# Kernel optimization log

Measured on AMD Instinct MI355X. Metric: run time of the kernel, lower is better.

Reference implementation:

```python
import jax, jax.numpy as jnp
import numpy as np

F_FIELDS = 39
VOCAB = 200000
EMB = 16
D1 = 32
BATCH = 16384


def setup_inputs() -> dict:
    key = jax.random.key(0)
    ks = jax.random.split(key, 12)
    Xi = jax.random.randint(ks[0], (BATCH, F_FIELDS, 1), 0, VOCAB, dtype=jnp.int64 if jax.config.jax_enable_x64 else jnp.int32)
    Xv = jax.random.uniform(ks[1], (BATCH, F_FIELDS), dtype=jnp.float32)
    # one table per field, all same vocab -> stacked [F, V, E]
    tables = jax.random.normal(ks[2], (F_FIELDS, VOCAB, EMB), dtype=jnp.float32) * 0.05
    W1 = jax.random.normal(ks[3], (D1, F_FIELDS, EMB), dtype=jnp.float32)   # first_order_weight
    Wi = jax.random.normal(ks[4], (D1, F_FIELDS, EMB), dtype=jnp.float32)   # inner_second_weight_emb
    lin1_w = jax.random.normal(ks[5], (32, 32), dtype=jnp.float32) * (1.0 / np.sqrt(32))
    lin1_b = jax.random.normal(ks[6], (32,), dtype=jnp.float32) * 0.01
    lin2_w = jax.random.normal(ks[7], (32, 32), dtype=jnp.float32) * (1.0 / np.sqrt(32))
    lin2_b = jax.random.normal(ks[8], (32,), dtype=jnp.float32) * 0.01
    last_w = jax.random.normal(ks[9], (1, 32), dtype=jnp.float32) * (1.0 / np.sqrt(32))
    last_b = jax.random.normal(ks[10], (1,), dtype=jnp.float32) * 0.01
    return {"Xi": Xi, "Xv": Xv, "tables": tables, "W1": W1, "Wi": Wi,
            "lin1_w": lin1_w, "lin1_b": lin1_b, "lin2_w": lin2_w, "lin2_b": lin2_b,
            "last_w": last_w, "last_b": last_b}


def reference(Xi, Xv, tables, W1, Wi, lin1_w, lin1_b, lin2_w, lin2_b, last_w, last_b):
    # Per-field embedding lookup; Xi[:, f, 0] indexes field f's table.
    idx = Xi[:, :, 0]                                   # [B, F]
    emb = tables[jnp.arange(F_FIELDS)[None, :], idx]    # [B, F, E]
    emb = emb * Xv[:, :, None]                          # scale by feature value
    # first-order product layer: sum_j <emb_j, w_{i,j}> for each output unit i
    first_order = jnp.einsum('bfe,dfe->bd', emb, W1)    # [B, D1]
    # inner-product term: (sum_j <emb_j, wi_{i,j}>)^2
    s = jnp.einsum('bfe,dfe->bd', emb, Wi)
    x = first_order + s * s                             # [B, D1]
    # deep MLP (relu, eval mode: no dropout; bias param in original is unused in forward)
    x = jax.nn.relu(x @ lin1_w.T + lin1_b)
    x = jax.nn.relu(x @ lin2_w.T + lin2_b)
    out = x @ last_w.T + last_b                         # [B, 1]
    return jnp.sum(out, axis=1)                         # [B]
```

## Files before the change

### kernel.cpp

```cpp
#include <hip/hip_runtime.h>
#include <stdint.h>
#include <stddef.h>

#define F_FIELDS 39
#define VOCAB    200000
#define EMB      16
#define BATCH    16384
#define MBLK     32
#define NOUT     64
#define KPAD     640
#define NCHUNK   10
#define KC       64
#define ASTR     88
#define BSTR     88
#define CSTR     68

typedef __attribute__((ext_vector_type(8))) short bf16x8;
typedef __attribute__((ext_vector_type(4))) float f32x4;

__device__ __forceinline__ unsigned short f2bf(float x) {
  union { float f; unsigned int u; } a; a.f = x;
  unsigned int r = (a.u + 0x7fffu + ((a.u >> 16) & 1u)) >> 16;
  return (unsigned short)r;
}
__device__ __forceinline__ float bf2f(unsigned short h) {
  union { unsigned int u; float f; } a; a.u = ((unsigned int)h) << 16;
  return a.f;
}

__global__ void prep_w(const float* __restrict__ W1, const float* __restrict__ Wi,
                       unsigned short* __restrict__ Wt) {
  int i = blockIdx.x * 256 + threadIdx.x;
  if (i >= NOUT * KPAD) return;
  int n = i / KPAD, k = i % KPAD;
  float v = 0.0f;
  if (k < F_FIELDS * EMB) v = (n < 32) ? W1[n * 624 + k] : Wi[(n - 32) * 624 + k];
  Wt[i] = f2bf(v);
}

__global__ __launch_bounds__(256) void pnn_main(
    const int* __restrict__ Xi, const float* __restrict__ Xv,
    const float* __restrict__ tables, const unsigned short* __restrict__ Wt,
    const float* __restrict__ lin1_w, const float* __restrict__ lin1_b,
    const float* __restrict__ lin2_w, const float* __restrict__ lin2_b,
    const float* __restrict__ last_w, const float* __restrict__ last_b,
    float* __restrict__ out)
{
  const int t    = threadIdx.x;
  const int wave = t >> 6, lane = t & 63;
  const int l15  = lane & 15, quad = lane >> 4;

  __shared__ unsigned short A_sh[MBLK * ASTR];
  __shared__ unsigned short Al_sh[MBLK * ASTR];
  __shared__ unsigned short B_sh[NOUT * BSTR];
  __shared__ float          C_sh[MBLK * CSTR];
  __shared__ float          X1_sh[MBLK * 36];
  __shared__ float          W_lds[2145];

  for (int i = t; i < 1024; i += 256) {
    W_lds[i]        = lin1_w[i];
    W_lds[1024 + i] = lin2_w[i];
  }
  if (t < 32) {
    W_lds[2048 + t] = lin1_b[t];
    W_lds[2080 + t] = lin2_b[t];
    W_lds[2112 + t] = last_w[t];
  }
  if (t == 0) W_lds[2144] = last_b[0];

  const int gm    = t & 31;
  const int gfl   = (t >> 5) & 3;
  const int ghalf = t >> 7;
  const int sample = blockIdx.x * MBLK + gm;

  int   idxs[NCHUNK];
  float xvs[NCHUNK];
#pragma unroll
  for (int c = 0; c < NCHUNK; ++c) {
    int f = c * 4 + gfl;
    bool v = (f < F_FIELDS);
    int g = sample * F_FIELDS + (v ? f : 0);
    idxs[c] = v ? Xi[g] : 0;
    xvs[c]  = v ? Xv[g] : 0.0f;
  }

  const int bn = t >> 2, bseg = t & 3;

  const int m_tile = wave & 1, n_half = wave >> 1;
  const int arow = m_tile * 16 + l15;
  const int nb0  = n_half * 32 + l15;

  f32x4 acc0 = {0.f, 0.f, 0.f, 0.f};
  f32x4 acc1 = {0.f, 0.f, 0.f, 0.f};

#pragma unroll
  for (int c = 0; c < NCHUNK; ++c) {
    {
      const uint4* src = (const uint4*)(Wt + bn * KPAD + c * KC + bseg * 16);
      uint4 w0 = src[0], w1 = src[1];
      uint4* dst = (uint4*)&B_sh[bn * BSTR + bseg * 16];
      dst[0] = w0; dst[1] = w1;
    }
    {
      int f = c * 4 + gfl;
      float4 v0 = {0.f,0.f,0.f,0.f}, v1 = {0.f,0.f,0.f,0.f};
      float xv = xvs[c];
      if (f < F_FIELDS) {
        const float* p = tables + ((size_t)f * VOCAB + (size_t)idxs[c]) * EMB + ghalf * 8;
        v0 = *(const float4*)p;
        v1 = *(const float4*)(p + 4);
      }
      float vals[8] = { v0.x * xv, v0.y * xv, v0.z * xv, v0.w * xv,
                        v1.x * xv, v1.y * xv, v1.z * xv, v1.w * xv };
      union { unsigned short us[8]; uint4 v; } hi, lo;
#pragma unroll
      for (int j = 0; j < 8; ++j) {
        unsigned short h = f2bf(vals[j]);
        hi.us[j] = h;
        lo.us[j] = f2bf(vals[j] - bf2f(h));
      }
      *(uint4*)&A_sh[gm * ASTR + gfl * 16 + ghalf * 8]  = hi.v;
      *(uint4*)&Al_sh[gm * ASTR + gfl * 16 + ghalf * 8] = lo.v;
    }
    __syncthreads();
#pragma unroll
    for (int kk = 0; kk < 2; ++kk) {
      bf16x8 ah = *(const bf16x8*)&A_sh[arow * ASTR + kk * 32 + quad * 8];
      bf16x8 al = *(const bf16x8*)&Al_sh[arow * ASTR + kk * 32 + quad * 8];
      bf16x8 b0 = *(const bf16x8*)&B_sh[nb0 * BSTR + kk * 32 + quad * 8];
      bf16x8 b1 = *(const bf16x8*)&B_sh[(nb0 + 16) * BSTR + kk * 32 + quad * 8];
      acc0 = __builtin_amdgcn_mfma_f32_16x16x32_bf16(ah, b0, acc0, 0, 0, 0);
      acc1 = __builtin_amdgcn_mfma_f32_16x16x32_bf16(ah, b1, acc1, 0, 0, 0);
      acc0 = __builtin_amdgcn_mfma_f32_16x16x32_bf16(al, b0, acc0, 0, 0, 0);
      acc1 = __builtin_amdgcn_mfma_f32_16x16x32_bf16(al, b1, acc1, 0, 0, 0);
    }
    __syncthreads();
  }

  {
    int row_base = m_tile * 16 + quad * 4;
    int col0 = n_half * 32 + l15;
#pragma unroll
    for (int r = 0; r < 4; ++r) {
      C_sh[(row_base + r) * CSTR + col0]      = acc0[r];
      C_sh[(row_base + r) * CSTR + col0 + 16] = acc1[r];
    }
  }
  __syncthreads();

  {
    int m = t >> 3, j0 = (t & 7) * 4;
#pragma unroll
    for (int j = 0; j < 4; ++j) {
      float fo = C_sh[m * CSTR + j0 + j];
      float s  = C_sh[m * CSTR + 32 + j0 + j];
      C_sh[m * CSTR + j0 + j] = fo + s * s;
    }
  }
  __syncthreads();

  {
    const int m = t >> 3, d0 = (t & 7) * 4;
    float a0 = W_lds[2048 + d0 + 0];
    float a1 = W_lds[2048 + d0 + 1];
    float a2 = W_lds[2048 + d0 + 2];
    float a3 = W_lds[2048 + d0 + 3];
#pragma unroll
    for (int j = 0; j < 32; ++j) {
      float xj = C_sh[m * CSTR + j];
      a0 = fmaf(W_lds[(d0 + 0) * 32 + j], xj, a0);
      a1 = fmaf(W_lds[(d0 + 1) * 32 + j], xj, a1);
      a2 = fmaf(W_lds[(d0 + 2) * 32 + j], xj, a2);
      a3 = fmaf(W_lds[(d0 + 3) * 32 + j], xj, a3);
    }
    X1_sh[m * 36 + d0 + 0] = fmaxf(a0, 0.0f);
    X1_sh[m * 36 + d0 + 1] = fmaxf(a1, 0.0f);
    X1_sh[m * 36 + d0 + 2] = fmaxf(a2, 0.0f);
    X1_sh[m * 36 + d0 + 3] = fmaxf(a3, 0.0f);
  }
  __syncthreads();

  {
    const int m = t >> 3, d0 = (t & 7) * 4;
    float a0 = W_lds[2080 + d0 + 0];
    float a1 = W_lds[2080 + d0 + 1];
    float a2 = W_lds[2080 + d0 + 2];
    float a3 = W_lds[2080 + d0 + 3];
#pragma unroll
    for (int j = 0; j < 32; ++j) {
      float xj = X1_sh[m * 36 + j];
      a0 = fmaf(W_lds[1024 + (d0 + 0) * 32 + j], xj, a0);
      a1 = fmaf(W_lds[1024 + (d0 + 1) * 32 + j], xj, a1);
      a2 = fmaf(W_lds[1024 + (d0 + 2) * 32 + j], xj, a2);
      a3 = fmaf(W_lds[1024 + (d0 + 3) * 32 + j], xj, a3);
    }
    C_sh[m * CSTR + 32 + d0 + 0] = fmaxf(a0, 0.0f);
    C_sh[m * CSTR + 32 + d0 + 1] = fmaxf(a1, 0.0f);
    C_sh[m * CSTR + 32 + d0 + 2] = fmaxf(a2, 0.0f);
    C_sh[m * CSTR + 32 + d0 + 3] = fmaxf(a3, 0.0f);
  }
  __syncthreads();

  if (t < MBLK) {
    float s = W_lds[2144];
#pragma unroll
    for (int j = 0; j < 32; ++j)
      s = fmaf(W_lds[2112 + j], C_sh[t * CSTR + 32 + j], s);
    out[blockIdx.x * MBLK + t] = s;
  }
}

extern "C" void kernel_launch(void* const* d_in, const int* in_sizes, int n_in,
                              void* d_out, int out_size, void* d_ws, size_t ws_size,
                              hipStream_t stream) {
  (void)in_sizes; (void)n_in; (void)out_size; (void)ws_size;
  const int*   Xi     = (const int*)d_in[0];
  const float* Xv     = (const float*)d_in[1];
  const float* tables = (const float*)d_in[2];
  const float* W1     = (const float*)d_in[3];
  const float* Wi     = (const float*)d_in[4];
  const float* l1w    = (const float*)d_in[5];
  const float* l1b    = (const float*)d_in[6];
  const float* l2w    = (const float*)d_in[7];
  const float* l2b    = (const float*)d_in[8];
  const float* lw     = (const float*)d_in[9];
  const float* lb     = (const float*)d_in[10];
  float* out = (float*)d_out;

  unsigned short* Wt = (unsigned short*)d_ws;

  prep_w<<<dim3((NOUT * KPAD + 255) / 256), dim3(256), 0, stream>>>(W1, Wi, Wt);
  pnn_main<<<dim3(BATCH / MBLK), dim3(256), 0, stream>>>(
      Xi, Xv, tables, Wt, l1w, l1b, l2w, l2b, lw, lb, out);
}
```

Baseline: 578.3 us.

## Stage Xi/Xv through LDS and prefetch all embedding gathers upfront

The kernel now loads each block's Xi and Xv rows into shared memory with coalesced reads instead of strided per-thread loads. It then issues all ten embedding-row gathers into registers before the MFMA loop, so the random table accesses are all in flight together rather than serialized behind each chunk's barriers. It also sets launch_bounds(256, 2) to cap register use. The cost is 80 extra VGPRs of prefetched data plus about 10 KB more LDS per block, which can lower occupancy or cause spills.

```diff
diff --git a/kernel.cpp b/kernel.cpp
--- a/kernel.cpp
+++ b/kernel.cpp
@@ -38,7 +38,7 @@
   Wt[i] = f2bf(v);
 }
 
-__global__ __launch_bounds__(256) void pnn_main(
+__global__ __launch_bounds__(256, 2) void pnn_main(
     const int* __restrict__ Xi, const float* __restrict__ Xv,
     const float* __restrict__ tables, const unsigned short* __restrict__ Wt,
     const float* __restrict__ lin1_w, const float* __restrict__ lin1_b,
@@ -50,6 +50,8 @@
   const int wave = t >> 6, lane = t & 63;
   const int l15  = lane & 15, quad = lane >> 4;
 
+  __shared__ int            Ix_sh[MBLK * F_FIELDS];
+  __shared__ float          Vx_sh[MBLK * F_FIELDS];
   __shared__ unsigned short A_sh[MBLK * ASTR];
   __shared__ unsigned short Al_sh[MBLK * ASTR];
   __shared__ unsigned short B_sh[NOUT * BSTR];
@@ -57,6 +59,13 @@
   __shared__ float          X1_sh[MBLK * 36];
   __shared__ float          W_lds[2145];
 
+  {
+    const int base = blockIdx.x * MBLK * F_FIELDS;
+    for (int i = t; i < MBLK * F_FIELDS; i += 256) {
+      Ix_sh[i] = Xi[base + i];
+      Vx_sh[i] = Xv[base + i];
+    }
+  }
   for (int i = t; i < 1024; i += 256) {
     W_lds[i]        = lin1_w[i];
     W_lds[1024 + i] = lin2_w[i];
@@ -67,21 +76,30 @@
     W_lds[2112 + t] = last_w[t];
   }
   if (t == 0) W_lds[2144] = last_b[0];
+  __syncthreads();
 
   const int gm    = t & 31;
   const int gfl   = (t >> 5) & 3;
   const int ghalf = t >> 7;
-  const int sample = blockIdx.x * MBLK + gm;
-
-  int   idxs[NCHUNK];
+
   float xvs[NCHUNK];
+  float4 g0[NCHUNK], g1[NCHUNK];
+
 #pragma unroll
   for (int c = 0; c < NCHUNK; ++c) {
     int f = c * 4 + gfl;
     bool v = (f < F_FIELDS);
-    int g = sample * F_FIELDS + (v ? f : 0);
-    idxs[c] = v ? Xi[g] : 0;
-    xvs[c]  = v ? Xv[g] : 0.0f;
+    int loc = gm * F_FIELDS + (v ? f : 0);
+    int idx = Ix_sh[loc];
+    xvs[c]  = v ? Vx_sh[loc] : 0.0f;
+    if (v) {
+      const float* p = tables + ((size_t)f * VOCAB + (size_t)idx) * EMB + ghalf * 8;
+      g0[c] = *(const float4*)p;
+      g1[c] = *(const float4*)(p + 4);
+    } else {
+      g0[c] = make_float4(0.f, 0.f, 0.f, 0.f);
+      g1[c] = make_float4(0.f, 0.f, 0.f, 0.f);
+    }
   }
 
   const int bn = t >> 2, bseg = t & 3;
@@ -102,16 +120,9 @@
       dst[0] = w0; dst[1] = w1;
     }
     {
-      int f = c * 4 + gfl;
-      float4 v0 = {0.f,0.f,0.f,0.f}, v1 = {0.f,0.f,0.f,0.f};
       float xv = xvs[c];
-      if (f < F_FIELDS) {
-        const float* p = tables + ((size_t)f * VOCAB + (size_t)idxs[c]) * EMB + ghalf * 8;
-        v0 = *(const float4*)p;
-        v1 = *(const float4*)(p + 4);
-      }
-      float vals[8] = { v0.x * xv, v0.y * xv, v0.z * xv, v0.w * xv,
-                        v1.x * xv, v1.y * xv, v1.z * xv, v1.w * xv };
+      float vals[8] = { g0[c].x * xv, g0[c].y * xv, g0[c].z * xv, g0[c].w * xv,
+                        g1[c].x * xv, g1[c].y * xv, g1[c].z * xv, g1[c].w * xv };
       union { unsigned short us[8]; uint4 v; } hi, lo;
 #pragma unroll
       for (int j = 0; j < 8; ++j) {
```

After: 584.4 us. No clear change (+1.1%).
